# Kernel optimization log

Hardware: AMD Instinct MI355X
Metric: run time of the kernel (lower is better)

## Reference

```python
import jax, jax.numpy as jnp
import numpy as np

NUM_HEADS = 8
HIDDEN_DIM = 64
N_REAL = 30000
N_VIRT = 2000
N_NODES = N_REAL + N_VIRT
N_EDGES = 512000
VOCAB = 100000


def setup_inputs() -> dict:
    key = jax.random.key(0)
    k1, k2, k3, k4, k5 = jax.random.split(key, 5)
    features = jax.random.normal(k1, (VOCAB, HIDDEN_DIM), dtype=jnp.float32)
    virtue_emb = jax.random.normal(k2, (N_VIRT, HIDDEN_DIM), dtype=jnp.float32)  # nn.Embedding weight ~ N(0,1)
    cnodes = jax.random.randint(k3, (N_REAL,), 0, VOCAB, dtype=jnp.int64)
    src = jax.random.randint(k4, (N_EDGES,), 0, N_NODES, dtype=jnp.int64)
    dst = jax.random.randint(k5, (N_EDGES,), 0, N_NODES, dtype=jnp.int64)
    vm_idx = jnp.arange(N_VIRT, dtype=jnp.int64) + N_REAL  # virtual nodes are appended after real nodes
    return {"features": features, "virtue_emb": virtue_emb, "cnodes": cnodes,
            "src": src, "dst": dst, "vm_idx": vm_idx}


def _edge_softmax(e, dst, n_nodes):
    # DGL edge_softmax: softmax over incoming edges of each destination node.
    m = jax.ops.segment_max(e, dst, num_segments=n_nodes)          # [N,H,1]
    ex = jnp.exp(e - m[dst])                                       # [E,H,1]
    s = jax.ops.segment_sum(ex, dst, num_segments=n_nodes)        # [N,H,1]
    return ex / s[dst]


def reference(features, virtue_emb, cnodes, src, dst, vm_idx):
    real_ndata = features[cnodes]                                  # [R,D] F.embedding
    ndata = jnp.concatenate([real_ndata, virtue_emb], axis=0)      # [N,D]
    n = ndata.shape[0]
    # agg_type='neighbor': cat([h]*H, dim=1).view(-1,H,D) == broadcast along head dim
    nft = jnp.broadcast_to(ndata[:, None, :], (n, NUM_HEADS, HIDDEN_DIM))
    e = jnp.ones((src.shape[0], NUM_HEADS, 1), dtype=ndata.dtype)
    eft = _edge_softmax(e, dst, n)                                 # [E,H,1]
    new_nft = jax.ops.segment_sum(nft[src] * eft, dst, num_segments=n)      # round 1: u_mul_e / sum
    final_nft = jax.ops.segment_sum(new_nft[src] * eft, dst, num_segments=n)  # round 2
    return final_nft[vm_idx]                                       # [V,H,D]
```

## Files before the change

### kernel.cpp

```cpp
#include <hip/hip_runtime.h>

constexpr int HEADS  = 8;
constexpr int DIM    = 64;
constexpr int NREAL  = 30000;
constexpr int NVIRT  = 2000;
constexpr int NNODES = NREAL + NVIRT;
constexpr int NEDGES = 512000;
constexpr int STRIDE = 64;

constexpr int NSTAGE  = 2000;
constexpr int NBINBLK = 250;
constexpr int NBIN    = 256;
constexpr int NPB     = 125;
constexpr int CAP     = 48;

typedef _Float16 half4 __attribute__((ext_vector_type(4)));


__global__ __launch_bounds__(256) void k_prep(const float* __restrict__ features,
                                              const float* __restrict__ virtue,
                                              const int* __restrict__ cnodes,
                                              const int* __restrict__ src,
                                              const int* __restrict__ dst,
                                              _Float16* __restrict__ ndata,
                                              unsigned short* __restrict__ gHist,
                                              unsigned int* __restrict__ part,
                                              unsigned int* __restrict__ mark32) {
  if (blockIdx.x < NSTAGE) {
    int i = blockIdx.x * 256 + threadIdx.x;
    int node = i >> 4;
    int q    = i & 15;
    const float4* srcp = (node < NREAL)
        ? (const float4*)(features + (long)cnodes[node] * DIM)
        : (const float4*)(virtue + (long)(node - NREAL) * DIM);
    float4 v = srcp[q];
    half4 h = { (_Float16)v.x, (_Float16)v.y, (_Float16)v.z, (_Float16)v.w };
    ((half4*)(ndata + (long)node * DIM))[q] = h;
    return;
  }

  __shared__ unsigned int hist[NBIN];
  __shared__ unsigned int cur[NBIN];
  int b   = blockIdx.x - NSTAGE;
  int tid = threadIdx.x;

  if (b < 32) {
    int t32 = b * 256 + tid;
    if (t32 < NNODES / 4) mark32[t32] = 0;
  }

  hist[tid] = 0;
  __syncthreads();

  int e0 = b * 2048 + tid * 8;
  int4 sa = *(const int4*)(src + e0);
  int4 sb = *(const int4*)(src + e0 + 4);
  int4 da = *(const int4*)(dst + e0);
  int4 db = *(const int4*)(dst + e0 + 4);
  int ds8[8] = { da.x, da.y, da.z, da.w, db.x, db.y, db.z, db.w };
  int ss8[8] = { sa.x, sa.y, sa.z, sa.w, sb.x, sb.y, sb.z, sb.w };
  int bn8[8];
#pragma unroll
  for (int j = 0; j < 8; ++j) {
    bn8[j] = ds8[j] / NPB;
    atomicAdd(&hist[bn8[j]], 1u);
  }
  __syncthreads();

  gHist[tid * 256 + b] = (unsigned short)hist[tid];
  cur[tid] = ((unsigned)tid * 256u + (unsigned)b) * CAP;
  __syncthreads();

#pragma unroll
  for (int j = 0; j < 8; ++j) {
    unsigned p   = atomicAdd(&cur[bn8[j]], 1u);
    unsigned lim = ((unsigned)bn8[j] * 256u + (unsigned)b) * CAP + CAP;
    if (p < lim)
      part[p] = ((unsigned)ds8[j] << 15) | (unsigned)ss8[j];
  }
}

__global__ __launch_bounds__(256) void k_bin2(const unsigned short* __restrict__ gHist,
                                              const unsigned int* __restrict__ part,
                                              int* __restrict__ cnt,
                                              unsigned char* __restrict__ mark,
                                              unsigned short* __restrict__ slots) {
  __shared__ unsigned short slotbuf[NPB * STRIDE];
  __shared__ int            cntloc[NPB];
  __shared__ unsigned int   pre[257];

  int B = blockIdx.x, tid = threadIdx.x;
  if (tid < NPB) cntloc[tid] = 0;

  unsigned c = (tid < NBINBLK) ? (unsigned)gHist[B * 256 + tid] : 0u;
  if (c > CAP) c = CAP;
  pre[tid + 1] = c;
  if (tid == 0) pre[0] = 0;
  __syncthreads();
  for (int off = 1; off < 256; off <<= 1) {
    unsigned v = 0;
    if (tid >= off) v = pre[tid + 1 - off];
    __syncthreads();
    pre[tid + 1] += v;
    __syncthreads();
  }
  unsigned T = pre[256];
  int base0 = B * NPB;

  for (unsigned t = tid; t < T; t += 256) {
    int lo = 0, hi = 255;
    while (lo < hi) { int mid = (lo + hi + 1) >> 1; if (pre[mid] <= t) lo = mid; else hi = mid - 1; }
    unsigned w = part[((unsigned)B * 256u + (unsigned)lo) * CAP + (t - pre[lo])];
    int d = (int)(w >> 15);
    int s = (int)(w & 0x7fffu);
    int r = d - base0;
    int pos = atomicAdd(&cntloc[r], 1);
    if (pos < STRIDE) slotbuf[r * STRIDE + pos] = (unsigned short)s;
    if (d >= NREAL) mark[s] = 1;
  }
  __syncthreads();

  unsigned int* gs = (unsigned int*)(slots + (long)base0 * STRIDE);
  const unsigned int* ls = (const unsigned int*)slotbuf;
  for (int k = tid; k < NPB * STRIDE / 2; k += 256) gs[k] = ls[k];
  if (tid < NPB) cnt[base0 + tid] = cntloc[tid];
}

__global__ __launch_bounds__(256) void k_agg1(const int* __restrict__ cnt,
                                              const unsigned char* __restrict__ mark,
                                              const unsigned short* __restrict__ slots,
                                              const _Float16* __restrict__ ndata,
                                              float* __restrict__ new_nft) {
  int node = blockIdx.x * 4 + (threadIdx.x >> 6);
  if (node >= NNODES) return;
  int lane = threadIdx.x & 63;
  int q = lane >> 4;
  int l = lane & 15;
  unsigned char m = mark[node];
  int deg = cnt[node];
  int myidx = (int)slots[(long)node * STRIDE + lane];
  if (!m) return;
  if (deg > STRIDE) deg = STRIDE;
  float4 acc  = make_float4(0.f, 0.f, 0.f, 0.f);
  float4 acc2 = make_float4(0.f, 0.f, 0.f, 0.f);
  const half4* nd = (const half4*)ndata;
#pragma unroll
  for (int u = 0; u < 8; ++u) {
    int ka = u * 8 + q;
    int kb = u * 8 + q + 4;
    int sa = __shfl(myidx, ka);
    int sb = __shfl(myidx, kb);
    if (ka < deg) {
      half4 v = nd[(long)sa * 16 + l];
      acc.x += (float)v.x; acc.y += (float)v.y; acc.z += (float)v.z; acc.w += (float)v.w;
    }
    if (kb < deg) {
      half4 v = nd[(long)sb * 16 + l];
      acc2.x += (float)v.x; acc2.y += (float)v.y; acc2.z += (float)v.z; acc2.w += (float)v.w;
    }
  }
  acc.x += acc2.x; acc.y += acc2.y; acc.z += acc2.z; acc.w += acc2.w;
  acc.x += __shfl_xor(acc.x, 16); acc.y += __shfl_xor(acc.y, 16);
  acc.z += __shfl_xor(acc.z, 16); acc.w += __shfl_xor(acc.w, 16);
  acc.x += __shfl_xor(acc.x, 32); acc.y += __shfl_xor(acc.y, 32);
  acc.z += __shfl_xor(acc.z, 32); acc.w += __shfl_xor(acc.w, 32);
  if (q == 0) {
    float inv = (deg > 0) ? 1.0f / (float)deg : 0.0f;
    acc.x *= inv; acc.y *= inv; acc.z *= inv; acc.w *= inv;
    ((float4*)new_nft)[(long)node * 16 + l] = acc;
  }
}

__global__ __launch_bounds__(256) void k_agg2(const int* __restrict__ cnt,
                                              const unsigned short* __restrict__ slots,
                                              const float* __restrict__ new_nft,
                                              float* __restrict__ out) {
  int v = blockIdx.x * 4 + (threadIdx.x >> 6);
  if (v >= NVIRT) return;
  int node = NREAL + v;
  int lane = threadIdx.x & 63;
  int q = lane >> 4;
  int l = lane & 15;
  int deg = cnt[node];
  int myidx = (int)slots[(long)node * STRIDE + lane];
  if (deg > STRIDE) deg = STRIDE;
  float4 acc  = make_float4(0.f, 0.f, 0.f, 0.f);
  float4 acc2 = make_float4(0.f, 0.f, 0.f, 0.f);
  const float4* nf4 = (const float4*)new_nft;
#pragma unroll
  for (int u = 0; u < 8; ++u) {
    int ka = u * 8 + q;
    int kb = u * 8 + q + 4;
    int sa = __shfl(myidx, ka);
    int sb = __shfl(myidx, kb);
    if (ka < deg) {
      float4 x = nf4[(long)sa * 16 + l];
      acc.x += x.x; acc.y += x.y; acc.z += x.z; acc.w += x.w;
    }
    if (kb < deg) {
      float4 x = nf4[(long)sb * 16 + l];
      acc2.x += x.x; acc2.y += x.y; acc2.z += x.z; acc2.w += x.w;
    }
  }
  acc.x += acc2.x; acc.y += acc2.y; acc.z += acc2.z; acc.w += acc2.w;
  acc.x += __shfl_xor(acc.x, 16); acc.y += __shfl_xor(acc.y, 16);
  acc.z += __shfl_xor(acc.z, 16); acc.w += __shfl_xor(acc.w, 16);
  acc.x += __shfl_xor(acc.x, 32); acc.y += __shfl_xor(acc.y, 32);
  acc.z += __shfl_xor(acc.z, 32); acc.w += __shfl_xor(acc.w, 32);
  if (q == 0) {
    float inv = (deg > 0) ? 1.0f / (float)deg : 0.0f;
    acc.x *= inv; acc.y *= inv; acc.z *= inv; acc.w *= inv;
    float4* o4 = (float4*)out;
#pragma unroll
    for (int h = 0; h < HEADS; ++h)
      o4[((long)v * HEADS + h) * 16 + l] = acc;
  }
}


extern "C" void kernel_launch(void* const* d_in, const int* in_sizes, int n_in,
                              void* d_out, int out_size, void* d_ws, size_t ws_size,
                              hipStream_t stream) {
  const float* features = (const float*)d_in[0];
  const float* virtue   = (const float*)d_in[1];
  const int*   cnodes   = (const int*)d_in[2];
  const int*   src      = (const int*)d_in[3];
  const int*   dst      = (const int*)d_in[4];
  float* out = (float*)d_out;

  float*          new_nft = (float*)d_ws;
  _Float16*       ndata   = (_Float16*)(new_nft + (long)NNODES * DIM);
  int*            cnt     = (int*)(ndata + (long)NNODES * DIM);
  unsigned char*  mark    = (unsigned char*)(cnt + NNODES);
  unsigned short* slots   = (unsigned short*)(mark + NNODES);
  unsigned short* gHist   = slots + (long)NNODES * STRIDE;
  unsigned int*   part    = (unsigned int*)(gHist + NBIN * 256);

  const int B = 256;

  k_prep<<<NSTAGE + NBINBLK, B, 0, stream>>>(features, virtue, cnodes, src, dst,
                                             ndata, gHist, part, (unsigned int*)mark);
  k_bin2<<<NBIN, B, 0, stream>>>(gHist, part, cnt, mark, slots);
  k_agg1<<<(NNODES + 3) / 4, B, 0, stream>>>(cnt, mark, slots, ndata, new_nft);
  k_agg2<<<(NVIRT + 3) / 4, B, 0, stream>>>(cnt, slots, new_nft, out);
}
```

Before: 121.6 us.

## Fuse binning with round-one aggregation and drop source-mark pruning

Merges the bin-scatter kernel and the first aggregation kernel into one 1024-thread kernel. Each block aggregates its 125 destination nodes straight from the shared-memory slot buffer and writes global slots and counts only for virtual nodes. This removes one launch and the global round trip of the slot lists. In exchange, the mark-based pruning is gone, so round one now aggregates every node instead of only sources that feed virtual nodes. Each block also loops over its nodes with only 16 waves across 256 blocks, which lowers parallelism in the gather phase.

```diff
diff --git a/kernel.cpp b/kernel.cpp
--- a/kernel.cpp
+++ b/kernel.cpp
@@ -24,8 +24,7 @@
                                               const int* __restrict__ dst,
                                               _Float16* __restrict__ ndata,
                                               unsigned short* __restrict__ gHist,
-                                              unsigned int* __restrict__ part,
-                                              unsigned int* __restrict__ mark32) {
+                                              unsigned int* __restrict__ part) {
   if (blockIdx.x < NSTAGE) {
     int i = blockIdx.x * 256 + threadIdx.x;
     int node = i >> 4;
@@ -44,11 +43,6 @@
   int b   = blockIdx.x - NSTAGE;
   int tid = threadIdx.x;
 
-  if (b < 32) {
-    int t32 = b * 256 + tid;
-    if (t32 < NNODES / 4) mark32[t32] = 0;
-  }
-
   hist[tid] = 0;
   __syncthreads();
 
@@ -80,11 +74,12 @@
   }
 }
 
-__global__ __launch_bounds__(256) void k_bin2(const unsigned short* __restrict__ gHist,
-                                              const unsigned int* __restrict__ part,
-                                              int* __restrict__ cnt,
-                                              unsigned char* __restrict__ mark,
-                                              unsigned short* __restrict__ slots) {
+__global__ __launch_bounds__(1024) void k_binagg(const unsigned short* __restrict__ gHist,
+                                                 const unsigned int* __restrict__ part,
+                                                 const _Float16* __restrict__ ndata,
+                                                 int* __restrict__ cnt,
+                                                 unsigned short* __restrict__ slots,
+                                                 float* __restrict__ new_nft) {
   __shared__ unsigned short slotbuf[NPB * STRIDE];
   __shared__ int            cntloc[NPB];
   __shared__ unsigned int   pre[257];
@@ -92,22 +87,24 @@
   int B = blockIdx.x, tid = threadIdx.x;
   if (tid < NPB) cntloc[tid] = 0;
 
-  unsigned c = (tid < NBINBLK) ? (unsigned)gHist[B * 256 + tid] : 0u;
-  if (c > CAP) c = CAP;
-  pre[tid + 1] = c;
-  if (tid == 0) pre[0] = 0;
+  if (tid < 256) {
+    unsigned c = (tid < NBINBLK) ? (unsigned)gHist[B * 256 + tid] : 0u;
+    if (c > CAP) c = CAP;
+    pre[tid + 1] = c;
+    if (tid == 0) pre[0] = 0;
+  }
   __syncthreads();
   for (int off = 1; off < 256; off <<= 1) {
     unsigned v = 0;
-    if (tid >= off) v = pre[tid + 1 - off];
+    if (tid >= off && tid < 256) v = pre[tid + 1 - off];
     __syncthreads();
-    pre[tid + 1] += v;
+    if (tid >= off && tid < 256) pre[tid + 1] += v;
     __syncthreads();
   }
   unsigned T = pre[256];
   int base0 = B * NPB;
 
-  for (unsigned t = tid; t < T; t += 256) {
+  for (unsigned t = tid; t < T; t += 1024) {
     int lo = 0, hi = 255;
     while (lo < hi) { int mid = (lo + hi + 1) >> 1; if (pre[mid] <= t) lo = mid; else hi = mid - 1; }
     unsigned w = part[((unsigned)B * 256u + (unsigned)lo) * CAP + (t - pre[lo])];
@@ -116,58 +113,53 @@
     int r = d - base0;
     int pos = atomicAdd(&cntloc[r], 1);
     if (pos < STRIDE) slotbuf[r * STRIDE + pos] = (unsigned short)s;
-    if (d >= NREAL) mark[s] = 1;
-  }
-  __syncthreads();
-
-  unsigned int* gs = (unsigned int*)(slots + (long)base0 * STRIDE);
-  const unsigned int* ls = (const unsigned int*)slotbuf;
-  for (int k = tid; k < NPB * STRIDE / 2; k += 256) gs[k] = ls[k];
-  if (tid < NPB) cnt[base0 + tid] = cntloc[tid];
-}
-
-__global__ __launch_bounds__(256) void k_agg1(const int* __restrict__ cnt,
-                                              const unsigned char* __restrict__ mark,
-                                              const unsigned short* __restrict__ slots,
-                                              const _Float16* __restrict__ ndata,
-                                              float* __restrict__ new_nft) {
-  int node = blockIdx.x * 4 + (threadIdx.x >> 6);
-  if (node >= NNODES) return;
-  int lane = threadIdx.x & 63;
+  }
+  __syncthreads();
+
+  int wave = tid >> 6;
+  int lane = tid & 63;
   int q = lane >> 4;
   int l = lane & 15;
-  unsigned char m = mark[node];
-  int deg = cnt[node];
-  int myidx = (int)slots[(long)node * STRIDE + lane];
-  if (!m) return;
-  if (deg > STRIDE) deg = STRIDE;
-  float4 acc  = make_float4(0.f, 0.f, 0.f, 0.f);
-  float4 acc2 = make_float4(0.f, 0.f, 0.f, 0.f);
   const half4* nd = (const half4*)ndata;
-#pragma unroll
-  for (int u = 0; u < 8; ++u) {
-    int ka = u * 8 + q;
-    int kb = u * 8 + q + 4;
-    int sa = __shfl(myidx, ka);
-    int sb = __shfl(myidx, kb);
-    if (ka < deg) {
-      half4 v = nd[(long)sa * 16 + l];
-      acc.x += (float)v.x; acc.y += (float)v.y; acc.z += (float)v.z; acc.w += (float)v.w;
-    }
-    if (kb < deg) {
-      half4 v = nd[(long)sb * 16 + l];
-      acc2.x += (float)v.x; acc2.y += (float)v.y; acc2.z += (float)v.z; acc2.w += (float)v.w;
-    }
-  }
-  acc.x += acc2.x; acc.y += acc2.y; acc.z += acc2.z; acc.w += acc2.w;
-  acc.x += __shfl_xor(acc.x, 16); acc.y += __shfl_xor(acc.y, 16);
-  acc.z += __shfl_xor(acc.z, 16); acc.w += __shfl_xor(acc.w, 16);
-  acc.x += __shfl_xor(acc.x, 32); acc.y += __shfl_xor(acc.y, 32);
-  acc.z += __shfl_xor(acc.z, 32); acc.w += __shfl_xor(acc.w, 32);
-  if (q == 0) {
-    float inv = (deg > 0) ? 1.0f / (float)deg : 0.0f;
-    acc.x *= inv; acc.y *= inv; acc.z *= inv; acc.w *= inv;
-    ((float4*)new_nft)[(long)node * 16 + l] = acc;
+  for (int r = wave; r < NPB; r += 16) {
+    int deg = cntloc[r];
+    if (deg > STRIDE) deg = STRIDE;
+    int myidx = (int)slotbuf[r * STRIDE + lane];
+    float4 acc  = make_float4(0.f, 0.f, 0.f, 0.f);
+    float4 acc2 = make_float4(0.f, 0.f, 0.f, 0.f);
+#pragma unroll
+    for (int u = 0; u < 8; ++u) {
+      int ka = u * 8 + q;
+      int kb = u * 8 + q + 4;
+      int sa = __shfl(myidx, ka);
+      int sb = __shfl(myidx, kb);
+      if (ka < deg) {
+        half4 v = nd[(long)sa * 16 + l];
+        acc.x += (float)v.x; acc.y += (float)v.y; acc.z += (float)v.z; acc.w += (float)v.w;
+      }
+      if (kb < deg) {
+        half4 v = nd[(long)sb * 16 + l];
+        acc2.x += (float)v.x; acc2.y += (float)v.y; acc2.z += (float)v.z; acc2.w += (float)v.w;
+      }
+    }
+    acc.x += acc2.x; acc.y += acc2.y; acc.z += acc2.z; acc.w += acc2.w;
+    acc.x += __shfl_xor(acc.x, 16); acc.y += __shfl_xor(acc.y, 16);
+    acc.z += __shfl_xor(acc.z, 16); acc.w += __shfl_xor(acc.w, 16);
+    acc.x += __shfl_xor(acc.x, 32); acc.y += __shfl_xor(acc.y, 32);
+    acc.z += __shfl_xor(acc.z, 32); acc.w += __shfl_xor(acc.w, 32);
+    if (q == 0) {
+      float inv = (deg > 0) ? 1.0f / (float)deg : 0.0f;
+      acc.x *= inv; acc.y *= inv; acc.z *= inv; acc.w *= inv;
+      ((float4*)new_nft)[(long)(base0 + r) * 16 + l] = acc;
+    }
+  }
+
+  if (base0 >= NREAL) {
+    int vbase = base0 - NREAL;
+    unsigned int* gs = (unsigned int*)(slots + (long)vbase * STRIDE);
+    const unsigned int* ls = (const unsigned int*)slotbuf;
+    for (int k2 = tid; k2 < NPB * STRIDE / 2; k2 += 1024) gs[k2] = ls[k2];
+    if (tid < NPB) cnt[vbase + tid] = cntloc[tid];
   }
 }
 
@@ -177,12 +169,11 @@
                                               float* __restrict__ out) {
   int v = blockIdx.x * 4 + (threadIdx.x >> 6);
   if (v >= NVIRT) return;
-  int node = NREAL + v;
   int lane = threadIdx.x & 63;
   int q = lane >> 4;
   int l = lane & 15;
-  int deg = cnt[node];
-  int myidx = (int)slots[(long)node * STRIDE + lane];
+  int deg = cnt[v];
+  int myidx = (int)slots[(long)v * STRIDE + lane];
   if (deg > STRIDE) deg = STRIDE;
   float4 acc  = make_float4(0.f, 0.f, 0.f, 0.f);
   float4 acc2 = make_float4(0.f, 0.f, 0.f, 0.f);
@@ -230,17 +221,15 @@
 
   float*          new_nft = (float*)d_ws;
   _Float16*       ndata   = (_Float16*)(new_nft + (long)NNODES * DIM);
-  int*            cnt     = (int*)(ndata + (long)NNODES * DIM);
-  unsigned char*  mark    = (unsigned char*)(cnt + NNODES);
-  unsigned short* slots   = (unsigned short*)(mark + NNODES);
-  unsigned short* gHist   = slots + (long)NNODES * STRIDE;
+  unsigned short* gHist   = (unsigned short*)(ndata + (long)NNODES * DIM);
   unsigned int*   part    = (unsigned int*)(gHist + NBIN * 256);
+  int*            cnt     = (int*)(part + (long)NBIN * 256 * CAP);
+  unsigned short* slots   = (unsigned short*)(cnt + NVIRT);
 
   const int B = 256;
 
   k_prep<<<NSTAGE + NBINBLK, B, 0, stream>>>(features, virtue, cnodes, src, dst,
-                                             ndata, gHist, part, (unsigned int*)mark);
-  k_bin2<<<NBIN, B, 0, stream>>>(gHist, part, cnt, mark, slots);
-  k_agg1<<<(NNODES + 3) / 4, B, 0, stream>>>(cnt, mark, slots, ndata, new_nft);
+                                             ndata, gHist, part);
+  k_binagg<<<NBIN, 1024, 0, stream>>>(gHist, part, ndata, cnt, slots, new_nft);
   k_agg2<<<(NVIRT + 3) / 4, B, 0, stream>>>(cnt, slots, new_nft, out);
 }
```

Result: no change. 119.9 us (-1.4%).
